# Kernel tuning notes

Measured on AMD Instinct MI355X. Metric: run time of the kernel, lower is better.

Reference implementation:

```python
import jax, jax.numpy as jnp
import numpy as np

N_NODES = 50000
N_EDGES = 800000
H_DIM = 128
HIDDEN = 256


def _glorot(key, shape):
    fan_in, fan_out = shape[1], shape[0]
    lim = np.sqrt(6.0 / (fan_in + fan_out)).astype(np.float32)
    return jax.random.uniform(key, shape, jnp.float32, -lim, lim)


def setup_inputs() -> dict:
    key = jax.random.key(0)
    ks = jax.random.split(key, 12)
    h = jax.random.normal(ks[0], (N_NODES, H_DIM), jnp.float32)
    coord_diff = jax.random.normal(ks[1], (N_EDGES, 3), jnp.float32)
    row = jax.random.randint(ks[2], (N_EDGES,), 0, N_NODES, jnp.int64)
    col = jax.random.randint(ks[3], (N_EDGES,), 0, N_NODES, jnp.int64)
    # edge MLP: Linear(2*H+1 -> HIDDEN), SiLU, Linear(HIDDEN -> HIDDEN), SiLU
    We1 = _glorot(ks[4], (HIDDEN, 2 * H_DIM + 1))
    be1 = jnp.zeros((HIDDEN,), jnp.float32)
    We2 = _glorot(ks[5], (HIDDEN, HIDDEN))
    be2 = jnp.zeros((HIDDEN,), jnp.float32)
    # node MLP: Linear(HIDDEN + H -> HIDDEN), SiLU, Linear(HIDDEN -> H)
    Wn1 = _glorot(ks[6], (HIDDEN, HIDDEN + H_DIM))
    bn1 = jnp.zeros((HIDDEN,), jnp.float32)
    Wn2 = _glorot(ks[7], (H_DIM, HIDDEN))
    bn2 = jnp.zeros((H_DIM,), jnp.float32)
    return {"h": h, "coord_diff": coord_diff, "row": row, "col": col,
            "We1": We1, "be1": be1, "We2": We2, "be2": be2,
            "Wn1": Wn1, "bn1": bn1, "Wn2": Wn2, "bn2": bn2}


def reference(h, coord_diff, row, col, We1, be1, We2, be2, Wn1, bn1, Wn2, bn2):
    # radial: squared edge length, [E, 1]
    radial = jnp.sum(coord_diff ** 2, axis=1, keepdims=True)
    # edge model: gather endpoints, concat, 2-layer SiLU MLP
    e_in = jnp.concatenate([h[row], h[col], radial], axis=1)  # [E, 2H+1]
    m = jax.nn.silu(e_in @ We1.T + be1)                        # [E, HIDDEN]
    m = jax.nn.silu(m @ We2.T + be2)                           # [E, HIDDEN]
    # node model: scatter-add messages to source node `row`
    agg = jax.ops.segment_sum(m, row, num_segments=h.shape[0])  # [N, HIDDEN]
    n_in = jnp.concatenate([h, agg], axis=1)                    # [N, HIDDEN+H]
    out = jax.nn.silu(n_in @ Wn1.T + bn1) @ Wn2.T + bn2         # [N, H]
    return out
```

## Files before the change

kernel.cpp:

```cpp
#include <hip/hip_runtime.h>
#include <cstdint>
#include <cstddef>

#define E_EDGES 800000
#define N_NODES 50000
#define HDIM 128
#define HID 256
#define ME 64
#define NB 64
#define NTILES 196

typedef __attribute__((ext_vector_type(8))) short short8;
typedef __attribute__((ext_vector_type(4))) float f32x4;

__device__ __forceinline__ float silu(float y) {
    return y * __builtin_amdgcn_rcpf(1.0f + __expf(-y));
}

__device__ __forceinline__ short f2bfn(float f) {
    __bf16 b = (__bf16)f;
    return __builtin_bit_cast(short, b);
}
__device__ __forceinline__ float bf2f(short s) {
    return __uint_as_float(((unsigned int)(unsigned short)s) << 16);
}

#define PREP_H    6250
#define PREP_AGG  (PREP_H + 12500)
#define PREP_HIST (PREP_AGG + 3125)
#define PREP_WE1  (PREP_HIST + 288)
#define PREP_WE2  (PREP_WE1 + 288)
#define PREP_WN1  (PREP_WE2 + 416)
#define PREP_WN2  (PREP_WN1 + 144)
__global__ void prep_kernel(const float* __restrict__ h, short* __restrict__ hbf,
                            float* __restrict__ agg,
                            const int* __restrict__ row, int* __restrict__ cnt,
                            const float* __restrict__ We1, const float* __restrict__ be1,
                            short* __restrict__ Wb1,
                            const float* __restrict__ We2, const float* __restrict__ be2,
                            short* __restrict__ Wb2,
                            const float* __restrict__ Wn1, const float* __restrict__ bn1,
                            short* __restrict__ Wbn1,
                            const float* __restrict__ Wn2, const float* __restrict__ bn2,
                            short* __restrict__ Wbn2) {
    const int b = blockIdx.x, t = threadIdx.x;
    if (b < PREP_H) {
        int i = b * 256 + t;
        float4 v = ((const float4*)h)[i];
        short4 s;
        s.x = f2bfn(v.x); s.y = f2bfn(v.y); s.z = f2bfn(v.z); s.w = f2bfn(v.w);
        ((short4*)hbf)[i] = s;
    } else if (b < PREP_AGG) {
        int i = (b - PREP_H) * 256 + t;
        ((float4*)agg)[i] = make_float4(0.f, 0.f, 0.f, 0.f);
    } else if (b < PREP_HIST) {
        int e = (b - PREP_AGG) * 256 + t;
        if (e < E_EDGES) atomicAdd(&cnt[row[e]], 1);
    } else if (b < PREP_WE1) {
        int idx = (b - PREP_HIST) * 256 + t;
        int c = idx / 288, k = idx - c * 288;
        short v = 0;
        if (k < 257)       v = f2bfn(We1[c * 257 + k]);
        else if (k == 257) v = f2bfn(be1[c]);
        Wb1[idx] = v;
    } else if (b < PREP_WE2) {
        int idx = (b - PREP_WE1) * 256 + t;
        int c = idx / 288, k = idx - c * 288;
        short v = 0;
        if (k < 256)       v = f2bfn(We2[c * 256 + k]);
        else if (k == 256) v = f2bfn(be2[c]);
        Wb2[idx] = v;
    } else if (b < PREP_WN1) {
        int idx = (b - PREP_WE2) * 256 + t;
        int c = idx / 416, k = idx - c * 416;
        short v = 0;
        if (k < 384)       v = f2bfn(Wn1[c * 384 + k]);
        else if (k == 384) v = f2bfn(bn1[c]);
        Wbn1[idx] = v;
    } else {
        int idx = (b - PREP_WN1) * 256 + t;
        int c = idx / 288, k = idx - c * 288;
        short v = 0;
        if (k < 256)       v = f2bfn(Wn2[c * 256 + k]);
        else if (k == 256) v = f2bfn(bn2[c]);
        Wbn2[idx] = v;
    }
}

__global__ void scanA_kernel(const int* __restrict__ cnt, int* __restrict__ incl,
                             int* __restrict__ tsum) {
    const int b = blockIdx.x, t = threadIdx.x;
    const int i = b * 256 + t;
    const int lane = t & 63, wv = t >> 6;
    int v = (i < N_NODES) ? cnt[i] : 0;
    int s = v;
#pragma unroll
    for (int off = 1; off < 64; off <<= 1) {
        int u = __shfl_up(s, off, 64);
        if (lane >= off) s += u;
    }
    __shared__ int wsum[4];
    if (lane == 63) wsum[wv] = s;
    __syncthreads();
    int pre = 0;
#pragma unroll
    for (int j = 0; j < 3; ++j) if (wv > j) pre += wsum[j];
    s += pre;
    if (i < N_NODES) incl[i] = s;
    if (t == 255) tsum[b] = s;
}

__global__ void scanB_kernel(const int* __restrict__ tsum, int* __restrict__ toff) {
    const int t = threadIdx.x;
    const int lane = t & 63, wv = t >> 6;
    int v = (t < NTILES) ? tsum[t] : 0;
    int s = v;
#pragma unroll
    for (int off = 1; off < 64; off <<= 1) {
        int u = __shfl_up(s, off, 64);
        if (lane >= off) s += u;
    }
    __shared__ int wsum[4];
    if (lane == 63) wsum[wv] = s;
    __syncthreads();
    int pre = 0;
#pragma unroll
    for (int j = 0; j < 3; ++j) if (wv > j) pre += wsum[j];
    s += pre;
    if (t < NTILES) toff[t] = s - v;
}

__global__ void scanC_kernel(const int* __restrict__ cnt, int* __restrict__ cursor,
                             const int* __restrict__ toff) {
    const int b = blockIdx.x, t = threadIdx.x;
    const int i = b * 256 + t;
    if (i < N_NODES) {
        cursor[i] = cursor[i] - cnt[i] + toff[b];
    }
}

__global__ void fill_kernel(const int* __restrict__ row, int* __restrict__ cursor,
                            int* __restrict__ eidx) {
    int e = blockIdx.x * 256 + threadIdx.x;
    if (e < E_EDGES) {
        int pos = atomicAdd(&cursor[row[e]], 1);
        eidx[pos] = e;
    }
}

__global__ __launch_bounds__(256, 4) void edge_kernel(
    const short* __restrict__ hb, const float* __restrict__ coord,
    const int* __restrict__ row, const int* __restrict__ col,
    const int* __restrict__ eidx,
    const short* __restrict__ Wb1, const short* __restrict__ Wb2,
    float* __restrict__ agg)
{
    __shared__ __align__(16) short shPool[ME * 256 + ME * 32];
    __shared__ int sr[ME];
    short* shA = shPool;
    short* shT = shPool + ME * 256;

    const int t = threadIdx.x;
    const int nwg = E_EDGES / ME;
    const int qq = nwg >> 3, rr = nwg & 7;
    const int xcd = blockIdx.x & 7, bi = blockIdx.x >> 3;
    const int wg = (xcd < rr ? xcd * (qq + 1) : rr * (qq + 1) + (xcd - rr) * qq) + bi;
    const int e0 = wg * ME;

    {
        const int e = t >> 2, q = t & 3;
        const int eo = eidx[e0 + e];
        const int src = (q < 2) ? row[eo] : col[eo];
        const short8* hp = (const short8*)(hb + (size_t)src * HDIM + (q & 1) * 64);
#pragma unroll
        for (int c = 0; c < 8; ++c) {
            short8 v = hp[c];
            int chunk = 8 * q + c;
            int sw = chunk ^ (e & 7);
            *(short8*)&shA[e * 256 + sw * 8] = v;
        }
        short8 z = {0, 0, 0, 0, 0, 0, 0, 0};
        if (q == 0) {
            float cx = coord[3 * eo + 0];
            float cy = coord[3 * eo + 1];
            float cz = coord[3 * eo + 2];
            z[0] = f2bfn(cx * cx + cy * cy + cz * cz);
            z[1] = (short)0x3F80;
            sr[e] = src;
        }
        *(short8*)&shT[e * 32 + ((q ^ (e & 3)) << 3)] = z;
    }
    __syncthreads();

    const int l = t & 63, w = t >> 6;
    const int l15 = l & 15, lq = l >> 4;

    f32x4 acc[4][4];
#pragma unroll
    for (int i = 0; i < 4; ++i)
#pragma unroll
        for (int j = 0; j < 4; ++j) acc[i][j] = (f32x4){0.f, 0.f, 0.f, 0.f};

#pragma unroll
    for (int ks = 0; ks < 8; ++ks) {
        short8 a[4], b[4];
#pragma unroll
        for (int et = 0; et < 4; ++et) {
            int r = et * 16 + l15;
            int chunk = ks * 4 + lq;
            a[et] = *(const short8*)&shA[r * 256 + ((chunk ^ (r & 7)) << 3)];
        }
#pragma unroll
        for (int ct = 0; ct < 4; ++ct) {
            int cc = w * 64 + ct * 16 + l15;
            b[ct] = *(const short8*)&Wb1[cc * 288 + ks * 32 + lq * 8];
        }
#pragma unroll
        for (int et = 0; et < 4; ++et)
#pragma unroll
            for (int ct = 0; ct < 4; ++ct)
                acc[et][ct] = __builtin_amdgcn_mfma_f32_16x16x32_bf16(
                    a[et], b[ct], acc[et][ct], 0, 0, 0);
    }
    {
        short8 a[4], b[4];
#pragma unroll
        for (int et = 0; et < 4; ++et) {
            int r = et * 16 + l15;
            a[et] = *(const short8*)&shT[r * 32 + ((lq ^ (r & 3)) << 3)];
        }
#pragma unroll
        for (int ct = 0; ct < 4; ++ct) {
            int cc = w * 64 + ct * 16 + l15;
            b[ct] = *(const short8*)&Wb1[cc * 288 + 256 + lq * 8];
        }
#pragma unroll
        for (int et = 0; et < 4; ++et)
#pragma unroll
            for (int ct = 0; ct < 4; ++ct)
                acc[et][ct] = __builtin_amdgcn_mfma_f32_16x16x32_bf16(
                    a[et], b[ct], acc[et][ct], 0, 0, 0);
    }
    __syncthreads();

    {
        if (t < ME) {
            *(unsigned int*)&shT[t * 32 + ((t & 3) << 3)] = 0x00003F80u;
        }
#pragma unroll
        for (int et = 0; et < 4; ++et) {
#pragma unroll
            for (int rp = 0; rp < 2; ++rp) {
                int er0 = et * 16 + lq * 4 + rp * 2;
#pragma unroll
                for (int ct = 0; ct < 4; ++ct) {
                    int kc = w * 64 + ct * 16 + l15;
                    float y0 = silu(acc[et][ct][rp * 2]);
                    float y1 = silu(acc[et][ct][rp * 2 + 1]);
                    int khi = kc >> 3, klo = kc & 7;
                    shA[er0 * 256 + ((khi ^ (er0 & 7)) << 3) + klo] = f2bfn(y0);
                    shA[(er0 + 1) * 256 + ((khi ^ ((er0 + 1) & 7)) << 3) + klo] = f2bfn(y1);
                }
            }
        }
    }
    __syncthreads();

#pragma unroll
    for (int i = 0; i < 4; ++i)
#pragma unroll
        for (int j = 0; j < 4; ++j) acc[i][j] = (f32x4){0.f, 0.f, 0.f, 0.f};
#pragma unroll
    for (int ks = 0; ks < 8; ++ks) {
        short8 a[4], b[4];
#pragma unroll
        for (int et = 0; et < 4; ++et) {
            int r = et * 16 + l15;
            int chunk = ks * 4 + lq;
            a[et] = *(const short8*)&shA[r * 256 + ((chunk ^ (r & 7)) << 3)];
        }
#pragma unroll
        for (int ct = 0; ct < 4; ++ct) {
            int cc = w * 64 + ct * 16 + l15;
            b[ct] = *(const short8*)&Wb2[cc * 288 + ks * 32 + lq * 8];
        }
#pragma unroll
        for (int et = 0; et < 4; ++et)
#pragma unroll
            for (int ct = 0; ct < 4; ++ct)
                acc[et][ct] = __builtin_amdgcn_mfma_f32_16x16x32_bf16(
                    a[et], b[ct], acc[et][ct], 0, 0, 0);
    }
    {
        short8 a[4], b[4];
#pragma unroll
        for (int et = 0; et < 4; ++et) {
            int r = et * 16 + l15;
            a[et] = *(const short8*)&shT[r * 32 + ((lq ^ (r & 3)) << 3)];
        }
#pragma unroll
        for (int ct = 0; ct < 4; ++ct) {
            int cc = w * 64 + ct * 16 + l15;
            b[ct] = *(const short8*)&Wb2[cc * 288 + 256 + lq * 8];
        }
#pragma unroll
        for (int et = 0; et < 4; ++et)
#pragma unroll
            for (int ct = 0; ct < 4; ++ct)
                acc[et][ct] = __builtin_amdgcn_mfma_f32_16x16x32_bf16(
                    a[et], b[ct], acc[et][ct], 0, 0, 0);
    }
    __syncthreads();

    {
#pragma unroll
        for (int ct = 0; ct < 4; ++ct) {
#pragma unroll
            for (int et = 0; et < 4; ++et) {
                int kc = w * 64 + ct * 16 + l15;
                int er0 = et * 16 + lq * 4;
                short4 s;
                s.x = f2bfn(silu(acc[et][ct][0]));
                s.y = f2bfn(silu(acc[et][ct][1]));
                s.z = f2bfn(silu(acc[et][ct][2]));
                s.w = f2bfn(silu(acc[et][ct][3]));
                *(short4*)&shPool[kc * 68 + er0] = s;
            }
        }
    }
    __syncthreads();

    {
        const int cc = t;
        const short* myrow = &shPool[cc * 68];
        float accum = 0.f;
        int cur = sr[0];
        for (int eb = 0; eb < ME; eb += 4) {
            short4 v4 = *(const short4*)&myrow[eb];
            short vj[4] = {v4.x, v4.y, v4.z, v4.w};
#pragma unroll
            for (int j = 0; j < 4; ++j) {
                float v = bf2f(vj[j]);
                int r = sr[eb + j];
                if (r != cur) {
                    atomicAdd(&agg[(size_t)cur * HID + cc], accum);
                    accum = v;
                    cur = r;
                } else {
                    accum += v;
                }
            }
        }
        atomicAdd(&agg[(size_t)cur * HID + cc], accum);
    }
}

__global__ __launch_bounds__(256, 3) void node_kernel(
    const short* __restrict__ hbf, const float* __restrict__ agg,
    const short* __restrict__ Wbn1, const short* __restrict__ Wbn2,
    float* __restrict__ out)
{
    __shared__ __align__(16) short pool[NB * 384];
    __shared__ __align__(16) short shTn[NB * 32];
    short* shH  = pool;
    short* shAg = pool + NB * 128;
    short* shM  = pool;

    const int t  = threadIdx.x;
    const int n0 = blockIdx.x * NB;

    {
        const int n = t >> 2, q = t & 3;
        int gn = n0 + n;
        if (gn >= N_NODES) gn = N_NODES - 1;
        const short8* hp = (const short8*)(hbf + (size_t)gn * HDIM + q * 32);
#pragma unroll
        for (int c = 0; c < 4; ++c) {
            short8 v = hp[c];
            int chunk = q * 4 + c;
            int sw = chunk ^ (n & 7);
            *(short8*)&shH[n * 128 + sw * 8] = v;
        }
        const float4* ap = (const float4*)(agg + (size_t)gn * HID + q * 64);
#pragma unroll
        for (int i = 0; i < 8; ++i) {
            float4 u0 = ap[2 * i], u1 = ap[2 * i + 1];
            short8 s;
            s[0] = f2bfn(u0.x); s[1] = f2bfn(u0.y); s[2] = f2bfn(u0.z); s[3] = f2bfn(u0.w);
            s[4] = f2bfn(u1.x); s[5] = f2bfn(u1.y); s[6] = f2bfn(u1.z); s[7] = f2bfn(u1.w);
            int chunk = q * 8 + i;
            int sw2 = chunk ^ (n & 7);
            *(short8*)&shAg[n * 256 + sw2 * 8] = s;
        }
        short8 z = {0, 0, 0, 0, 0, 0, 0, 0};
        if (q == 0) z[0] = (short)0x3F80;
        *(short8*)&shTn[n * 32 + ((q ^ (n & 3)) << 3)] = z;
    }
    __syncthreads();

    const int l = t & 63, w = t >> 6;
    const int l15 = l & 15, lq = l >> 4;

    f32x4 acc[4][4];
#pragma unroll
    for (int i = 0; i < 4; ++i)
#pragma unroll
        for (int j = 0; j < 4; ++j) acc[i][j] = (f32x4){0.f, 0.f, 0.f, 0.f};
#pragma unroll
    for (int ks = 0; ks < 12; ++ks) {
        short8 a[4], b[4];
#pragma unroll
        for (int et = 0; et < 4; ++et) {
            int r = et * 16 + l15;
            if (ks < 4) {
                int chunk = ks * 4 + lq;
                a[et] = *(const short8*)&shH[r * 128 + ((chunk ^ (r & 7)) << 3)];
            } else {
                int chunk = (ks - 4) * 4 + lq;
                a[et] = *(const short8*)&shAg[r * 256 + ((chunk ^ (r & 7)) << 3)];
            }
        }
#pragma unroll
        for (int ct = 0; ct < 4; ++ct) {
            int cc = w * 64 + ct * 16 + l15;
            b[ct] = *(const short8*)&Wbn1[cc * 416 + ks * 32 + lq * 8];
        }
#pragma unroll
        for (int et = 0; et < 4; ++et)
#pragma unroll
            for (int ct = 0; ct < 4; ++ct)
                acc[et][ct] = __builtin_amdgcn_mfma_f32_16x16x32_bf16(
                    a[et], b[ct], acc[et][ct], 0, 0, 0);
    }
    {
        short8 a[4], b[4];
#pragma unroll
        for (int et = 0; et < 4; ++et) {
            int r = et * 16 + l15;
            a[et] = *(const short8*)&shTn[r * 32 + ((lq ^ (r & 3)) << 3)];
        }
#pragma unroll
        for (int ct = 0; ct < 4; ++ct) {
            int cc = w * 64 + ct * 16 + l15;
            b[ct] = *(const short8*)&Wbn1[cc * 416 + 384 + lq * 8];
        }
#pragma unroll
        for (int et = 0; et < 4; ++et)
#pragma unroll
            for (int ct = 0; ct < 4; ++ct)
                acc[et][ct] = __builtin_amdgcn_mfma_f32_16x16x32_bf16(
                    a[et], b[ct], acc[et][ct], 0, 0, 0);
    }
    __syncthreads();

    {
#pragma unroll
        for (int et = 0; et < 4; ++et) {
#pragma unroll
            for (int rp = 0; rp < 2; ++rp) {
                int er0 = et * 16 + lq * 4 + rp * 2;
#pragma unroll
                for (int ct = 0; ct < 4; ++ct) {
                    int kc = w * 64 + ct * 16 + l15;
                    float y0 = silu(acc[et][ct][rp * 2]);
                    float y1 = silu(acc[et][ct][rp * 2 + 1]);
                    int khi = kc >> 3, klo = kc & 7;
                    shM[er0 * 256 + ((khi ^ (er0 & 7)) << 3) + klo] = f2bfn(y0);
                    shM[(er0 + 1) * 256 + ((khi ^ ((er0 + 1) & 7)) << 3) + klo] = f2bfn(y1);
                }
            }
        }
    }
    __syncthreads();

    f32x4 acc2[4][2];
#pragma unroll
    for (int i = 0; i < 4; ++i)
#pragma unroll
        for (int j = 0; j < 2; ++j) acc2[i][j] = (f32x4){0.f, 0.f, 0.f, 0.f};
#pragma unroll
    for (int ks = 0; ks < 8; ++ks) {
        short8 a[4], b2[2];
#pragma unroll
        for (int et = 0; et < 4; ++et) {
            int r = et * 16 + l15;
            int chunk = ks * 4 + lq;
            a[et] = *(const short8*)&shM[r * 256 + ((chunk ^ (r & 7)) << 3)];
        }
#pragma unroll
        for (int ct = 0; ct < 2; ++ct) {
            int cc = w * 32 + ct * 16 + l15;
            b2[ct] = *(const short8*)&Wbn2[cc * 288 + ks * 32 + lq * 8];
        }
#pragma unroll
        for (int et = 0; et < 4; ++et)
#pragma unroll
            for (int ct = 0; ct < 2; ++ct)
                acc2[et][ct] = __builtin_amdgcn_mfma_f32_16x16x32_bf16(
                    a[et], b2[ct], acc2[et][ct], 0, 0, 0);
    }
    {
        short8 a[4], b2[2];
#pragma unroll
        for (int et = 0; et < 4; ++et) {
            int r = et * 16 + l15;
            a[et] = *(const short8*)&shTn[r * 32 + ((lq ^ (r & 3)) << 3)];
        }
#pragma unroll
        for (int ct = 0; ct < 2; ++ct) {
            int cc = w * 32 + ct * 16 + l15;
            b2[ct] = *(const short8*)&Wbn2[cc * 288 + 256 + lq * 8];
        }
#pragma unroll
        for (int et = 0; et < 4; ++et)
#pragma unroll
            for (int ct = 0; ct < 2; ++ct)
                acc2[et][ct] = __builtin_amdgcn_mfma_f32_16x16x32_bf16(
                    a[et], b2[ct], acc2[et][ct], 0, 0, 0);
    }

#pragma unroll
    for (int et = 0; et < 4; ++et) {
#pragma unroll
        for (int ct = 0; ct < 2; ++ct) {
            int cc = w * 32 + ct * 16 + l15;
#pragma unroll
            for (int r4 = 0; r4 < 4; ++r4) {
                int gn = n0 + et * 16 + lq * 4 + r4;
                if (gn < N_NODES)
                    out[(size_t)gn * HDIM + cc] = acc2[et][ct][r4];
            }
        }
    }
}

extern "C" void kernel_launch(void* const* d_in, const int* in_sizes, int n_in,
                              void* d_out, int out_size, void* d_ws, size_t ws_size,
                              hipStream_t stream) {
    const float* h   = (const float*)d_in[0];
    const float* cd  = (const float*)d_in[1];
    const int*   row = (const int*)d_in[2];
    const int*   col = (const int*)d_in[3];
    const float* We1 = (const float*)d_in[4];
    const float* be1 = (const float*)d_in[5];
    const float* We2 = (const float*)d_in[6];
    const float* be2 = (const float*)d_in[7];
    const float* Wn1 = (const float*)d_in[8];
    const float* bn1 = (const float*)d_in[9];
    const float* Wn2 = (const float*)d_in[10];
    const float* bn2 = (const float*)d_in[11];
    float* out = (float*)d_out;

    short* Wb1  = (short*)d_ws;
    short* Wb2  = Wb1 + 256 * 288;
    short* Wbn1 = Wb2 + 256 * 288;
    short* Wbn2 = Wbn1 + 256 * 416;
    short* hbf  = Wbn2 + 128 * 288;
    float* agg  = (float*)(hbf + (size_t)N_NODES * HDIM);
    int*   cnt    = (int*)(agg + (size_t)N_NODES * HID);
    int*   cursor = cnt + N_NODES;
    int*   eidx   = cursor + N_NODES;
    int*   tsum   = eidx + E_EDGES;
    int*   toff   = tsum + 256;

    hipMemsetAsync(cnt, 0, N_NODES * sizeof(int), stream);

    prep_kernel<<<PREP_WN2, 256, 0, stream>>>(h, hbf, agg, row, cnt,
                                              We1, be1, Wb1, We2, be2, Wb2,
                                              Wn1, bn1, Wbn1, Wn2, bn2, Wbn2);

    scanA_kernel<<<NTILES, 256, 0, stream>>>(cnt, cursor, tsum);
    scanB_kernel<<<1, 256, 0, stream>>>(tsum, toff);
    scanC_kernel<<<NTILES, 256, 0, stream>>>(cnt, cursor, toff);
    fill_kernel<<<(E_EDGES + 255) / 256, 256, 0, stream>>>(row, cursor, eidx);

    edge_kernel<<<E_EDGES / ME, 256, 0, stream>>>(hbf, cd, row, col, eidx,
                                                  Wb1, Wb2, agg);
    node_kernel<<<(N_NODES + NB - 1) / NB, 256, 0, stream>>>(hbf, agg, Wbn1, Wbn2, out);
}
```

Measured before the change: 487.7 us.

## Precompute per-node first-layer projections to remove edge-level first GEMM

The first edge linear layer is split by linearity: a new kernel computes h@W_a^T+b and h@W_b^T for every node once (50k nodes instead of 800k edges). The edge kernel then gathers the two bf16 256-wide projections, adds radial*w_r, and applies SiLU before the second GEMM. This removes one large MFMA GEMM per edge but doubles the gathered bytes per edge (512 bf16 values instead of 256) and adds a workspace buffer plus an extra rounding step. It also adds MFMA priority hints and readfirstlane on the segment-row loads.

```diff
diff --git a/kernel.cpp b/kernel.cpp
--- a/kernel.cpp
+++ b/kernel.cpp
@@ -28,15 +28,16 @@
 #define PREP_H    6250
 #define PREP_AGG  (PREP_H + 12500)
 #define PREP_HIST (PREP_AGG + 3125)
-#define PREP_WE1  (PREP_HIST + 288)
-#define PREP_WE2  (PREP_WE1 + 288)
+#define PREP_WAB  (PREP_HIST + 320)
+#define PREP_WRF  (PREP_WAB + 1)
+#define PREP_WE2  (PREP_WRF + 288)
 #define PREP_WN1  (PREP_WE2 + 416)
 #define PREP_WN2  (PREP_WN1 + 144)
 __global__ void prep_kernel(const float* __restrict__ h, short* __restrict__ hbf,
                             float* __restrict__ agg,
                             const int* __restrict__ row, int* __restrict__ cnt,
                             const float* __restrict__ We1, const float* __restrict__ be1,
-                            short* __restrict__ Wb1,
+                            short* __restrict__ Wab, float* __restrict__ wrf,
                             const float* __restrict__ We2, const float* __restrict__ be2,
                             short* __restrict__ Wb2,
                             const float* __restrict__ Wn1, const float* __restrict__ bn1,
@@ -56,15 +57,21 @@
     } else if (b < PREP_HIST) {
         int e = (b - PREP_AGG) * 256 + t;
         if (e < E_EDGES) atomicAdd(&cnt[row[e]], 1);
-    } else if (b < PREP_WE1) {
+    } else if (b < PREP_WAB) {
         int idx = (b - PREP_HIST) * 256 + t;
-        int c = idx / 288, k = idx - c * 288;
+        int c = idx / 160, k = idx - c * 160;
         short v = 0;
-        if (k < 257)       v = f2bfn(We1[c * 257 + k]);
-        else if (k == 257) v = f2bfn(be1[c]);
-        Wb1[idx] = v;
+        if (c < 256) {
+            if (k < 128)       v = f2bfn(We1[c * 257 + k]);
+            else if (k == 128) v = f2bfn(be1[c]);
+        } else {
+            if (k < 128)       v = f2bfn(We1[(c - 256) * 257 + 128 + k]);
+        }
+        Wab[idx] = v;
+    } else if (b < PREP_WRF) {
+        wrf[t] = We1[t * 257 + 256];
     } else if (b < PREP_WE2) {
-        int idx = (b - PREP_WE1) * 256 + t;
+        int idx = (b - PREP_WRF) * 256 + t;
         int c = idx / 288, k = idx - c * 288;
         short v = 0;
         if (k < 256)       v = f2bfn(We2[c * 256 + k]);
@@ -148,12 +155,90 @@
     }
 }
 
+__global__ __launch_bounds__(256, 4) void hab_kernel(
+    const short* __restrict__ hbf, const short* __restrict__ Wab,
+    short* __restrict__ hab)
+{
+    __shared__ __align__(16) short shH[NB * 128];
+    __shared__ __align__(16) short shTh[NB * 32];
+
+    const int t = threadIdx.x;
+    const int tile = blockIdx.x >> 1;
+    const int half = blockIdx.x & 1;
+    const int n0 = tile * NB;
+
+    {
+        const int n = t >> 2, q = t & 3;
+        int gn = n0 + n;
+        if (gn >= N_NODES) gn = N_NODES - 1;
+        const short8* hp = (const short8*)(hbf + (size_t)gn * HDIM + q * 32);
+#pragma unroll
+        for (int c = 0; c < 4; ++c) {
+            short8 v = hp[c];
+            int chunk = q * 4 + c;
+            *(short8*)&shH[n * 128 + ((chunk ^ (n & 7)) << 3)] = v;
+        }
+        short8 z = {0, 0, 0, 0, 0, 0, 0, 0};
+        if (q == 0) z[0] = (short)0x3F80;
+        *(short8*)&shTh[n * 32 + ((q ^ (n & 3)) << 3)] = z;
+    }
+    __syncthreads();
+
+    const int l = t & 63, w = t >> 6;
+    const int l15 = l & 15, lq = l >> 4;
+
+    f32x4 acc[4][4];
+#pragma unroll
+    for (int i = 0; i < 4; ++i)
+#pragma unroll
+        for (int j = 0; j < 4; ++j) acc[i][j] = (f32x4){0.f, 0.f, 0.f, 0.f};
+
+#pragma unroll
+    for (int ks = 0; ks < 5; ++ks) {
+        short8 a[4], b[4];
+#pragma unroll
+        for (int et = 0; et < 4; ++et) {
+            int r = et * 16 + l15;
+            if (ks < 4) {
+                int chunk = ks * 4 + lq;
+                a[et] = *(const short8*)&shH[r * 128 + ((chunk ^ (r & 7)) << 3)];
+            } else {
+                a[et] = *(const short8*)&shTh[r * 32 + ((lq ^ (r & 3)) << 3)];
+            }
+        }
+#pragma unroll
+        for (int ct = 0; ct < 4; ++ct) {
+            int cc = half * 256 + w * 64 + ct * 16 + l15;
+            b[ct] = *(const short8*)&Wab[cc * 160 + ks * 32 + lq * 8];
+        }
+#pragma unroll
+        for (int et = 0; et < 4; ++et)
+#pragma unroll
+            for (int ct = 0; ct < 4; ++ct)
+                acc[et][ct] = __builtin_amdgcn_mfma_f32_16x16x32_bf16(
+                    a[et], b[ct], acc[et][ct], 0, 0, 0);
+    }
+
+#pragma unroll
+    for (int et = 0; et < 4; ++et) {
+#pragma unroll
+        for (int ct = 0; ct < 4; ++ct) {
+            int cc = half * 256 + w * 64 + ct * 16 + l15;
+#pragma unroll
+            for (int r4 = 0; r4 < 4; ++r4) {
+                int gn = n0 + et * 16 + lq * 4 + r4;
+                if (gn < N_NODES)
+                    hab[(size_t)gn * 512 + cc] = f2bfn(acc[et][ct][r4]);
+            }
+        }
+    }
+}
+
 __global__ __launch_bounds__(256, 4) void edge_kernel(
-    const short* __restrict__ hb, const float* __restrict__ coord,
+    const short* __restrict__ hab, const float* __restrict__ coord,
     const int* __restrict__ row, const int* __restrict__ col,
-    const int* __restrict__ eidx,
-    const short* __restrict__ Wb1, const short* __restrict__ Wb2,
-    float* __restrict__ agg)
+    const int* __restrict__ eidx, const float* __restrict__ wrf,
+    const short* __restrict__ Wb2, float* __restrict__ agg)
 {
     __shared__ __align__(16) short shPool[ME * 256 + ME * 32];
     __shared__ int sr[ME];
@@ -170,23 +255,38 @@
     {
         const int e = t >> 2, q = t & 3;
         const int eo = eidx[e0 + e];
-        const int src = (q < 2) ? row[eo] : col[eo];
-        const short8* hp = (const short8*)(hb + (size_t)src * HDIM + (q & 1) * 64);
-#pragma unroll
-        for (int c = 0; c < 8; ++c) {
-            short8 v = hp[c];
-            int chunk = 8 * q + c;
-            int sw = chunk ^ (e & 7);
-            *(short8*)&shA[e * 256 + sw * 8] = v;
+        const int rsrc = row[eo];
+        const int csrc = col[eo];
+        float cx = coord[3 * eo + 0];
+        float cy = coord[3 * eo + 1];
+        float cz = coord[3 * eo + 2];
+        float radial = cx * cx + cy * cy + cz * cz;
+        const short8* Ap = (const short8*)(hab + (size_t)rsrc * 512 + q * 64);
+        const short8* Bp = (const short8*)(hab + (size_t)csrc * 512 + 256 + q * 64);
+        const f32x4* Wp = (const f32x4*)(wrf + q * 64);
+#pragma unroll
+        for (int j = 0; j < 8; ++j) {
+            short8 av = Ap[j];
+            short8 bv = Bp[j];
+            f32x4 w0 = Wp[2 * j], w1 = Wp[2 * j + 1];
+            short8 o;
+#pragma unroll
+            for (int u = 0; u < 4; ++u) {
+                float y = bf2f(av[u]) + bf2f(bv[u]) + radial * w0[u];
+                o[u] = f2bfn(silu(y));
+            }
+#pragma unroll
+            for (int u = 0; u < 4; ++u) {
+                float y = bf2f(av[4 + u]) + bf2f(bv[4 + u]) + radial * w1[u];
+                o[4 + u] = f2bfn(silu(y));
+            }
+            int chunk = q * 8 + j;
+            *(short8*)&shA[e * 256 + ((chunk ^ (e & 7)) << 3)] = o;
         }
         short8 z = {0, 0, 0, 0, 0, 0, 0, 0};
         if (q == 0) {
-            float cx = coord[3 * eo + 0];
-            float cy = coord[3 * eo + 1];
-            float cz = coord[3 * eo + 2];
-            z[0] = f2bfn(cx * cx + cy * cy + cz * cz);
-            z[1] = (short)0x3F80;
-            sr[e] = src;
+            z[0] = (short)0x3F80;
+            sr[e] = rsrc;
         }
         *(short8*)&shT[e * 32 + ((q ^ (e & 3)) << 3)] = z;
     }
@@ -200,7 +300,6 @@
     for (int i = 0; i < 4; ++i)
 #pragma unroll
         for (int j = 0; j < 4; ++j) acc[i][j] = (f32x4){0.f, 0.f, 0.f, 0.f};
-
 #pragma unroll
     for (int ks = 0; ks < 8; ++ks) {
         short8 a[4], b[4];
@@ -213,14 +312,16 @@
 #pragma unroll
         for (int ct = 0; ct < 4; ++ct) {
             int cc = w * 64 + ct * 16 + l15;
-            b[ct] = *(const short8*)&Wb1[cc * 288 + ks * 32 + lq * 8];
-        }
+            b[ct] = *(const short8*)&Wb2[cc * 288 + ks * 32 + lq * 8];
+        }
+        __builtin_amdgcn_s_setprio(1);
 #pragma unroll
         for (int et = 0; et < 4; ++et)
 #pragma unroll
             for (int ct = 0; ct < 4; ++ct)
                 acc[et][ct] = __builtin_amdgcn_mfma_f32_16x16x32_bf16(
                     a[et], b[ct], acc[et][ct], 0, 0, 0);
+        __builtin_amdgcn_s_setprio(0);
     }
     {
         short8 a[4], b[4];
@@ -232,83 +333,16 @@
 #pragma unroll
         for (int ct = 0; ct < 4; ++ct) {
             int cc = w * 64 + ct * 16 + l15;
-            b[ct] = *(const short8*)&Wb1[cc * 288 + 256 + lq * 8];
-        }
+            b[ct] = *(const short8*)&Wb2[cc * 288 + 256 + lq * 8];
+        }
+        __builtin_amdgcn_s_setprio(1);
 #pragma unroll
         for (int et = 0; et < 4; ++et)
 #pragma unroll
             for (int ct = 0; ct < 4; ++ct)
                 acc[et][ct] = __builtin_amdgcn_mfma_f32_16x16x32_bf16(
                     a[et], b[ct], acc[et][ct], 0, 0, 0);
-    }
-    __syncthreads();
-
-    {
-        if (t < ME) {
-            *(unsigned int*)&shT[t * 32 + ((t & 3) << 3)] = 0x00003F80u;
-        }
-#pragma unroll
-        for (int et = 0; et < 4; ++et) {
-#pragma unroll
-            for (int rp = 0; rp < 2; ++rp) {
-                int er0 = et * 16 + lq * 4 + rp * 2;
-#pragma unroll
-                for (int ct = 0; ct < 4; ++ct) {
-                    int kc = w * 64 + ct * 16 + l15;
-                    float y0 = silu(acc[et][ct][rp * 2]);
-                    float y1 = silu(acc[et][ct][rp * 2 + 1]);
-                    int khi = kc >> 3, klo = kc & 7;
-                    shA[er0 * 256 + ((khi ^ (er0 & 7)) << 3) + klo] = f2bfn(y0);
-                    shA[(er0 + 1) * 256 + ((khi ^ ((er0 + 1) & 7)) << 3) + klo] = f2bfn(y1);
-                }
-            }
-        }
-    }
-    __syncthreads();
-
-#pragma unroll
-    for (int i = 0; i < 4; ++i)
-#pragma unroll
-        for (int j = 0; j < 4; ++j) acc[i][j] = (f32x4){0.f, 0.f, 0.f, 0.f};
-#pragma unroll
-    for (int ks = 0; ks < 8; ++ks) {
-        short8 a[4], b[4];
-#pragma unroll
-        for (int et = 0; et < 4; ++et) {
-            int r = et * 16 + l15;
-            int chunk = ks * 4 + lq;
-            a[et] = *(const short8*)&shA[r * 256 + ((chunk ^ (r & 7)) << 3)];
-        }
-#pragma unroll
-        for (int ct = 0; ct < 4; ++ct) {
-            int cc = w * 64 + ct * 16 + l15;
-            b[ct] = *(const short8*)&Wb2[cc * 288 + ks * 32 + lq * 8];
-        }
-#pragma unroll
-        for (int et = 0; et < 4; ++et)
-#pragma unroll
-            for (int ct = 0; ct < 4; ++ct)
-                acc[et][ct] = __builtin_amdgcn_mfma_f32_16x16x32_bf16(
-                    a[et], b[ct], acc[et][ct], 0, 0, 0);
-    }
-    {
-        short8 a[4], b[4];
-#pragma unroll
-        for (int et = 0; et < 4; ++et) {
-            int r = et * 16 + l15;
-            a[et] = *(const short8*)&shT[r * 32 + ((lq ^ (r & 3)) << 3)];
-        }
-#pragma unroll
-        for (int ct = 0; ct < 4; ++ct) {
-            int cc = w * 64 + ct * 16 + l15;
-            b[ct] = *(const short8*)&Wb2[cc * 288 + 256 + lq * 8];
-        }
-#pragma unroll
-        for (int et = 0; et < 4; ++et)
-#pragma unroll
-            for (int ct = 0; ct < 4; ++ct)
-                acc[et][ct] = __builtin_amdgcn_mfma_f32_16x16x32_bf16(
-                    a[et], b[ct], acc[et][ct], 0, 0, 0);
+        __builtin_amdgcn_s_setprio(0);
     }
     __syncthreads();
 
@@ -334,14 +368,14 @@
         const int cc = t;
         const short* myrow = &shPool[cc * 68];
         float accum = 0.f;
-        int cur = sr[0];
+        int cur = __builtin_amdgcn_readfirstlane(sr[0]);
         for (int eb = 0; eb < ME; eb += 4) {
             short4 v4 = *(const short4*)&myrow[eb];
             short vj[4] = {v4.x, v4.y, v4.z, v4.w};
 #pragma unroll
             for (int j = 0; j < 4; ++j) {
                 float v = bf2f(vj[j]);
-                int r = sr[eb + j];
+                int r = __builtin_amdgcn_readfirstlane(sr[eb + j]);
                 if (r != cur) {
                     atomicAdd(&agg[(size_t)cur * HID + cc], accum);
                     accum = v;
@@ -551,12 +585,14 @@
     const float* bn2 = (const float*)d_in[11];
     float* out = (float*)d_out;
 
-    short* Wb1  = (short*)d_ws;
-    short* Wb2  = Wb1 + 256 * 288;
+    short* Wab  = (short*)d_ws;
+    short* Wb2  = Wab + 512 * 160;
     short* Wbn1 = Wb2 + 256 * 288;
     short* Wbn2 = Wbn1 + 256 * 416;
-    short* hbf  = Wbn2 + 128 * 288;
-    float* agg  = (float*)(hbf + (size_t)N_NODES * HDIM);
+    float* wrf  = (float*)(Wbn2 + 128 * 288);
+    short* hbf  = (short*)(wrf + 256);
+    short* hab  = hbf + (size_t)N_NODES * HDIM;
+    float* agg  = (float*)(hab + (size_t)N_NODES * 512);
     int*   cnt    = (int*)(agg + (size_t)N_NODES * HID);
     int*   cursor = cnt + N_NODES;
     int*   eidx   = cursor + N_NODES;
@@ -566,15 +602,18 @@
     hipMemsetAsync(cnt, 0, N_NODES * sizeof(int), stream);
 
     prep_kernel<<<PREP_WN2, 256, 0, stream>>>(h, hbf, agg, row, cnt,
-                                              We1, be1, Wb1, We2, be2, Wb2,
+                                              We1, be1, Wab, wrf,
+                                              We2, be2, Wb2,
                                               Wn1, bn1, Wbn1, Wn2, bn2, Wbn2);
+
+    hab_kernel<<<((N_NODES + NB - 1) / NB) * 2, 256, 0, stream>>>(hbf, Wab, hab);
 
     scanA_kernel<<<NTILES, 256, 0, stream>>>(cnt, cursor, tsum);
     scanB_kernel<<<1, 256, 0, stream>>>(tsum, toff);
     scanC_kernel<<<NTILES, 256, 0, stream>>>(cnt, cursor, toff);
     fill_kernel<<<(E_EDGES + 255) / 256, 256, 0, stream>>>(row, cursor, eidx);
 
-    edge_kernel<<<E_EDGES / ME, 256, 0, stream>>>(hbf, cd, row, col, eidx,
-                                                  Wb1, Wb2, agg);
+    edge_kernel<<<E_EDGES / ME, 256, 0, stream>>>(hab, cd, row, col, eidx, wrf,
+                                                  Wb2, agg);
     node_kernel<<<(N_NODES + NB - 1) / NB, 256, 0, stream>>>(hbf, agg, Wbn1, Wbn2, out);
 }
```

After: 492.4 us. About the same (+1.0%).
